# Performance work log

Hardware: AMD Instinct MI355X
Metric: run time of the kernel (lower is better)

Reference implementation:

```python
import jax, jax.numpy as jnp
import numpy as np

B, S, H, E, K, D = 1, 4096, 1024, 8, 2, 2048

def setup_inputs() -> dict:
    key = jax.random.key(0)
    k1, k2, k3, k4, k5 = jax.random.split(key, 5)
    x = jax.random.normal(k1, (B, S, H), dtype=jnp.float32)
    attention_mask = jnp.ones((B, S), dtype=jnp.int32)
    expert_weights = jax.random.uniform(k2, (B, S, K), dtype=jnp.float32)
    # distinct top-K expert indices per token (torch code requires at most one match per token)
    r = jax.random.uniform(k3, (B, S, E))
    chosen_expert_indices = jnp.argsort(r, axis=-1)[..., :K].astype(jnp.int64)
    down_proj = jax.random.normal(k4, (E, H, D), dtype=jnp.float32)
    up_proj = jax.random.normal(k5, (E, D, H), dtype=jnp.float32)
    return {"x": x, "attention_mask": attention_mask, "expert_weights": expert_weights,
            "chosen_expert_indices": chosen_expert_indices, "down_proj": down_proj, "up_proj": up_proj}

def reference(x, attention_mask, expert_weights, chosen_expert_indices, down_proj, up_proj):
    b, s, h = x.shape
    e = down_proj.shape[0]
    xt = x.reshape(-1, h)                                   # [N,H]
    n = xt.shape[0]
    mask = attention_mask.reshape(n, 1).astype(x.dtype)     # [N,1]
    idx = chosen_expert_indices.reshape(n, -1)              # [N,K]
    w = expert_weights.reshape(n, -1)                       # [N,K]
    onehot = jax.nn.one_hot(idx, e, dtype=x.dtype)          # [N,K,E]
    # per-token routing weight for each expert (0 if not chosen), masked
    we = jnp.einsum('nk,nke->ne', w, onehot) * mask         # [N,E]
    hid = jax.nn.relu(jnp.einsum('nh,ehd->end', xt, down_proj))  # [E,N,D]
    y = jnp.einsum('end,edh->enh', hid, up_proj)            # [E,N,H]
    mlp = jnp.einsum('ne,enh->nh', we, y)                   # [N,H]
    out = xt + mlp                                          # residual (B==1 as in source)
    return out.reshape(b, s, h)
```

## Files before the change

kernel.cpp:

```cpp
#include <hip/hip_runtime.h>
#include <stdint.h>

#define NTOK 4096
#define HDIM 1024
#define DDIM 2048
#define NEXP 8
#define NASS 8192

typedef __attribute__((ext_vector_type(8))) short bf16x8;
typedef __attribute__((ext_vector_type(4))) float f32x4;

typedef __attribute__((address_space(1))) const unsigned int gu32;
typedef __attribute__((address_space(3))) unsigned int lu32;

#define BARRIER() asm volatile("s_barrier" ::: "memory")
#define WAIT_VM0() asm volatile("s_waitcnt vmcnt(0)" ::: "memory")
#define WAIT_LGKM0() do { asm volatile("s_waitcnt lgkmcnt(0)" ::: "memory"); \
                          __builtin_amdgcn_sched_barrier(0); } while (0)

__device__ __forceinline__ void async16(void* lds, const void* g) {
  __builtin_amdgcn_global_load_lds((gu32*)(uintptr_t)g, (lu32*)(uintptr_t)lds, 16, 0, 0);
}

__device__ __forceinline__ unsigned short f2bf(float f) {
  unsigned int u = __float_as_uint(f);
  return (unsigned short)((u + 0x7fffu + ((u >> 16) & 1u)) >> 16);
}
__device__ __forceinline__ float bf2f(unsigned short u) {
  return __uint_as_float(((unsigned int)u) << 16);
}
__device__ __forceinline__ unsigned int pack2(float lo, float hi) {
  return (unsigned int)f2bf(lo) | ((unsigned int)f2bf(hi) << 16);
}

__device__ __forceinline__ void transpose128(const float* __restrict__ in,
                                             unsigned short* __restrict__ out,
                                             int R, int C, int e, int bk, int bn,
                                             float* tile, int tid) {
  const size_t mbase = (size_t)e * R * C;
#pragma unroll
  for (int it = 0; it < 16; ++it) {
    int row = it * 8 + (tid >> 5);
    int c4 = (tid & 31) * 4;
    float4 v = *reinterpret_cast<const float4*>(
        in + mbase + (size_t)(bk * 128 + row) * C + bn * 128 + c4);
    tile[row * 129 + c4 + 0] = v.x; tile[row * 129 + c4 + 1] = v.y;
    tile[row * 129 + c4 + 2] = v.z; tile[row * 129 + c4 + 3] = v.w;
  }
  __syncthreads();
#pragma unroll
  for (int it = 0; it < 8; ++it) {
    int n = it * 16 + (tid >> 4);
    int k8 = (tid & 15) * 8;
    uint4 o;
    o.x = pack2(tile[(k8 + 0) * 129 + n], tile[(k8 + 1) * 129 + n]);
    o.y = pack2(tile[(k8 + 2) * 129 + n], tile[(k8 + 3) * 129 + n]);
    o.z = pack2(tile[(k8 + 4) * 129 + n], tile[(k8 + 5) * 129 + n]);
    o.w = pack2(tile[(k8 + 6) * 129 + n], tile[(k8 + 7) * 129 + n]);
    *reinterpret_cast<uint4*>(out + mbase + (size_t)(bn * 128 + n) * R + bk * 128 + k8) = o;
  }
}

__global__ __launch_bounds__(256) void k_prep(
    const float* __restrict__ x, unsigned short* __restrict__ x16,
    const float* __restrict__ dn, unsigned short* __restrict__ dnT,
    const float* __restrict__ up, unsigned short* __restrict__ upT) {
  __shared__ float tile[128 * 129];
  const int b = blockIdx.x;
  const int tid = threadIdx.x;
  if (b < 1024) {
    int e = b >> 7, t = b & 127;
    transpose128(dn, dnT, HDIM, DDIM, e, t & 7, t >> 3, tile, tid);
  } else if (b < 2048) {
    int idx = b - 1024;
    int e = idx >> 7, t = idx & 127;
    transpose128(up, upT, DDIM, HDIM, e, t & 15, t >> 4, tile, tid);
  } else {
    int i = (b - 2048) * 2048 + tid * 8;
    float4 v0 = *reinterpret_cast<const float4*>(x + i);
    float4 v1 = *reinterpret_cast<const float4*>(x + i + 4);
    uint4 o;
    o.x = pack2(v0.x, v0.y); o.y = pack2(v0.z, v0.w);
    o.z = pack2(v1.x, v1.y); o.w = pack2(v1.z, v1.w);
    *reinterpret_cast<uint4*>(x16 + i) = o;
  }
}

__global__ __launch_bounds__(1024) void k_route(
    const int* __restrict__ idx, const float* __restrict__ ew,
    const int* __restrict__ amask,
    int* __restrict__ counts_g, int* __restrict__ offs_g,
    int* __restrict__ toks, float* __restrict__ wl, int* __restrict__ slotmap) {
  __shared__ int cnt[NEXP], cur[NEXP], flag;
  const int t = threadIdx.x;
  if (t < NEXP) cnt[t] = 0;
  if (t == 0) flag = 0;
  __syncthreads();
  int lf = 0;
#pragma unroll
  for (int j = 0; j < 4; ++j) {
    int i = t + j * 1024;
    if (idx[2 * i + 1] != 0) lf = 1;
  }
  if (lf) atomicOr(&flag, 1);
  __syncthreads();
  const int is32 = flag;
  int e[8];
#pragma unroll
  for (int j = 0; j < 8; ++j) {
    int i = t + j * 1024;
    int ei = is32 ? idx[i] : idx[2 * i];
    e[j] = ei;
    atomicAdd(&cnt[ei], 1);
  }
  __syncthreads();
  if (t == 0) {
    int off = 0;
    for (int k = 0; k < NEXP; ++k) {
      cur[k] = off; offs_g[k] = off; counts_g[k] = cnt[k]; off += cnt[k];
    }
  }
  __syncthreads();
#pragma unroll
  for (int j = 0; j < 8; ++j) {
    int i = t + j * 1024;
    int n = i >> 1;
    int slot = atomicAdd(&cur[e[j]], 1);
    toks[slot] = n;
    wl[slot] = ew[i] * (amask[n] ? 1.0f : 0.0f);
    slotmap[i] = slot;
  }
}

__global__ __launch_bounds__(256, 4) void k_gemm_down(
    const unsigned short* __restrict__ x16, const unsigned short* __restrict__ bT,
    const int* __restrict__ counts, const int* __restrict__ offs,
    const int* __restrict__ toks, unsigned short* __restrict__ hid) {
  const int e = blockIdx.x;
  const int cnt = counts[e];
  const int q = blockIdx.y;
  const int mt = q >> 4;
  const int nt = q & 15;
  if (mt * 128 >= cnt) return;
  const int base = offs[e];
  __shared__ alignas(16) char lds[65536];
  const int tid = threadIdx.x;
  const int lane = tid & 63;
  const int wr = ((tid >> 7) & 1) * 64;
  const int wc = ((tid >> 6) & 1) * 64;

  const char* gA[4]; const char* gB[4]; int sOff[4];
  {
    const int swcol = ((tid & 7) << 4) ^ (((tid >> 3) & 7) << 4);
#pragma unroll
    for (int s = 0; s < 4; ++s) {
      int row = s * 32 + (tid >> 3);
      int sl = mt * 128 + row; if (sl >= cnt) sl = cnt - 1;
      gA[s] = (const char*)(x16 + (size_t)toks[base + sl] * HDIM) + swcol;
      gB[s] = (const char*)(bT + (size_t)e * DDIM * HDIM + (size_t)(nt * 128 + row) * HDIM) + swcol;
      sOff[s] = s * 4096 + tid * 16;
    }
  }
  const int swz = (lane & 7) << 4;
  const int lo = (lane >> 4) << 4;
  int rowA[4], rowB[4];
#pragma unroll
  for (int m = 0; m < 4; ++m) rowA[m] = (wr + m * 16 + (lane & 15)) * 128;
#pragma unroll
  for (int n = 0; n < 4; ++n) rowB[n] = (wc + n * 16 + (lane & 15)) * 128;

#pragma unroll
  for (int s = 0; s < 4; ++s) {
    async16(lds + sOff[s], gA[s]);
    async16(lds + 32768 + sOff[s], gB[s]);
  }

  f32x4 acc[4][4] = {};
  for (int j = 0; j < 16; ++j) {
    WAIT_VM0();
    BARRIER();
    char* curA = lds + ((j & 1) << 14);
    char* curB = lds + 32768 + ((j & 1) << 14);
    if (j < 15) {
      const int ko = (j + 1) << 7;
      char* nA = lds + ((~j & 1) << 14);
      char* nB = lds + 32768 + ((~j & 1) << 14);
#pragma unroll
      for (int s = 0; s < 4; ++s) {
        async16(nA + sOff[s], gA[s] + ko);
        async16(nB + sOff[s], gB[s] + ko);
      }
    }
#pragma unroll
    for (int ks = 0; ks < 2; ++ks) {
      const int cx = ((ks << 6) | lo) ^ swz;
      bf16x8 fa[4], fb[4];
#pragma unroll
      for (int n = 0; n < 4; ++n) fb[n] = *reinterpret_cast<const bf16x8*>(curB + rowB[n] + cx);
#pragma unroll
      for (int m = 0; m < 4; ++m) fa[m] = *reinterpret_cast<const bf16x8*>(curA + rowA[m] + cx);
      WAIT_LGKM0();
      __builtin_amdgcn_s_setprio(1);
#pragma unroll
      for (int m = 0; m < 4; ++m)
#pragma unroll
        for (int n = 0; n < 4; ++n)
          acc[m][n] = __builtin_amdgcn_mfma_f32_16x16x32_bf16(fa[m], fb[n], acc[m][n], 0, 0, 0);
      __builtin_amdgcn_s_setprio(0);
    }
  }

#pragma unroll
  for (int m = 0; m < 4; ++m) {
    int r0 = mt * 128 + wr + m * 16 + ((lane >> 4) * 4);
#pragma unroll
    for (int jj = 0; jj < 4; ++jj) {
      int r = r0 + jj;
      if (r < cnt) {
        unsigned short* dst = hid + (size_t)(base + r) * DDIM + nt * 128 + wc + (lane & 15);
#pragma unroll
        for (int n = 0; n < 4; ++n) {
          float v = acc[m][n][jj];
          dst[n * 16] = f2bf(v > 0.f ? v : 0.f);
        }
      }
    }
  }
}

__global__ __launch_bounds__(256, 4) void k_gemm_up(
    const unsigned short* __restrict__ hid, const unsigned short* __restrict__ bT,
    const int* __restrict__ counts, const int* __restrict__ offs,
    unsigned short* __restrict__ yw) {
  const int e = blockIdx.x;
  const int cnt = counts[e];
  const int q = blockIdx.y;
  const int mt = q >> 3;
  const int nt = q & 7;
  if (mt * 128 >= cnt) return;
  const int base = offs[e];
  __shared__ alignas(16) char lds[65536];
  const int tid = threadIdx.x;
  const int lane = tid & 63;
  const int wr = ((tid >> 7) & 1) * 64;
  const int wc = ((tid >> 6) & 1) * 64;

  const char* gA[4]; const char* gB[4]; int sOff[4];
  {
    const int swcol = ((tid & 7) << 4) ^ (((tid >> 3) & 7) << 4);
#pragma unroll
    for (int s = 0; s < 4; ++s) {
      int row = s * 32 + (tid >> 3);
      int sl = mt * 128 + row; if (sl >= cnt) sl = cnt - 1;
      gA[s] = (const char*)(hid + (size_t)(base + sl) * DDIM) + swcol;
      gB[s] = (const char*)(bT + (size_t)e * HDIM * DDIM + (size_t)(nt * 128 + row) * DDIM) + swcol;
      sOff[s] = s * 4096 + tid * 16;
    }
  }
  const int swz = (lane & 7) << 4;
  const int lo = (lane >> 4) << 4;
  int rowA[4], rowB[4];
#pragma unroll
  for (int m = 0; m < 4; ++m) rowA[m] = (wr + m * 16 + (lane & 15)) * 128;
#pragma unroll
  for (int n = 0; n < 4; ++n) rowB[n] = (wc + n * 16 + (lane & 15)) * 128;

#pragma unroll
  for (int s = 0; s < 4; ++s) {
    async16(lds + sOff[s], gA[s]);
    async16(lds + 32768 + sOff[s], gB[s]);
  }

  f32x4 acc[4][4] = {};
  for (int j = 0; j < 32; ++j) {
    WAIT_VM0();
    BARRIER();
    char* curA = lds + ((j & 1) << 14);
    char* curB = lds + 32768 + ((j & 1) << 14);
    if (j < 31) {
      const int ko = (j + 1) << 7;
      char* nA = lds + ((~j & 1) << 14);
      char* nB = lds + 32768 + ((~j & 1) << 14);
#pragma unroll
      for (int s = 0; s < 4; ++s) {
        async16(nA + sOff[s], gA[s] + ko);
        async16(nB + sOff[s], gB[s] + ko);
      }
    }
#pragma unroll
    for (int ks = 0; ks < 2; ++ks) {
      const int cx = ((ks << 6) | lo) ^ swz;
      bf16x8 fa[4], fb[4];
#pragma unroll
      for (int n = 0; n < 4; ++n) fb[n] = *reinterpret_cast<const bf16x8*>(curB + rowB[n] + cx);
#pragma unroll
      for (int m = 0; m < 4; ++m) fa[m] = *reinterpret_cast<const bf16x8*>(curA + rowA[m] + cx);
      WAIT_LGKM0();
      __builtin_amdgcn_s_setprio(1);
#pragma unroll
      for (int m = 0; m < 4; ++m)
#pragma unroll
        for (int n = 0; n < 4; ++n)
          acc[m][n] = __builtin_amdgcn_mfma_f32_16x16x32_bf16(fa[m], fb[n], acc[m][n], 0, 0, 0);
      __builtin_amdgcn_s_setprio(0);
    }
  }

#pragma unroll
  for (int m = 0; m < 4; ++m) {
    int r0 = mt * 128 + wr + m * 16 + ((lane >> 4) * 4);
#pragma unroll
    for (int jj = 0; jj < 4; ++jj) {
      int r = r0 + jj;
      if (r < cnt) {
        unsigned short* dst = yw + (size_t)(base + r) * HDIM + nt * 128 + wc + (lane & 15);
#pragma unroll
        for (int n = 0; n < 4; ++n) dst[n * 16] = f2bf(acc[m][n][jj]);
      }
    }
  }
}

__global__ __launch_bounds__(256) void k_combine(
    const float* __restrict__ x, const unsigned short* __restrict__ yw,
    const int* __restrict__ slotmap, const float* __restrict__ wl,
    float* __restrict__ out) {
  const int n = blockIdx.x;
  const int t = threadIdx.x;
  const int s0 = slotmap[2 * n], s1 = slotmap[2 * n + 1];
  const float w0 = wl[s0], w1 = wl[s1];
  float4 xv = reinterpret_cast<const float4*>(x + (size_t)n * HDIM)[t];
  ushort4 a0 = reinterpret_cast<const ushort4*>(yw + (size_t)s0 * HDIM)[t];
  ushort4 b0 = reinterpret_cast<const ushort4*>(yw + (size_t)s1 * HDIM)[t];
  float4 r;
  r.x = xv.x + w0 * bf2f(a0.x) + w1 * bf2f(b0.x);
  r.y = xv.y + w0 * bf2f(a0.y) + w1 * bf2f(b0.y);
  r.z = xv.z + w0 * bf2f(a0.z) + w1 * bf2f(b0.z);
  r.w = xv.w + w0 * bf2f(a0.w) + w1 * bf2f(b0.w);
  reinterpret_cast<float4*>(out + (size_t)n * HDIM)[t] = r;
}

extern "C" void kernel_launch(void* const* d_in, const int* in_sizes, int n_in,
                              void* d_out, int out_size, void* d_ws, size_t ws_size,
                              hipStream_t stream) {
  const float* x    = (const float*)d_in[0];
  const int* amask  = (const int*)d_in[1];
  const float* ew   = (const float*)d_in[2];
  const int* cidx   = (const int*)d_in[3];
  const float* dn   = (const float*)d_in[4];
  const float* up   = (const float*)d_in[5];
  float* out        = (float*)d_out;
  char* ws          = (char*)d_ws;

  const size_t X16_OFF = 0;
  const size_t DNT_OFF = X16_OFF + (size_t)NTOK * HDIM * 2;
  const size_t UPT_OFF = DNT_OFF + (size_t)NEXP * HDIM * DDIM * 2;
  const size_t HID_OFF = UPT_OFF + (size_t)NEXP * HDIM * DDIM * 2;
  const size_t MET_OFF = HID_OFF + (size_t)NASS * DDIM * 2;

  unsigned short* x16 = (unsigned short*)(ws + X16_OFF);
  unsigned short* dnT = (unsigned short*)(ws + DNT_OFF);
  unsigned short* upT = (unsigned short*)(ws + UPT_OFF);
  unsigned short* hid = (unsigned short*)(ws + HID_OFF);
  unsigned short* yw  = (unsigned short*)(ws + DNT_OFF);
  int* counts  = (int*)(ws + MET_OFF);
  int* offs    = counts + 8;
  int* toks    = counts + 32;
  float* wl    = (float*)(toks + NASS);
  int* slotmap = (int*)(wl + NASS);

  k_prep<<<1024 + 1024 + 2048, 256, 0, stream>>>(x, x16, dn, dnT, up, upT);
  k_route<<<1, 1024, 0, stream>>>(cidx, ew, amask, counts, offs, toks, wl, slotmap);
  k_gemm_down<<<dim3(8, 1024), 256, 0, stream>>>(x16, dnT, counts, offs, toks, hid);
  k_gemm_up<<<dim3(8, 512), 256, 0, stream>>>(hid, upT, counts, offs, yw);
  k_combine<<<NTOK, 256, 0, stream>>>(x, yw, slotmap, wl, out);
}
```

Measured before the change: 147.2 us.

## Fuse fp32 weight transpose and bf16 conversion into the expert GEMM B-tile loads

Removes the separate prep pass that transposed and converted both expert weight tensors to bf16. Each GEMM block now reads fp32 weights straight from global memory into registers, converts them to bf16 and writes them transposed into swizzled LDS, prefetching two K-tiles ahead. This saves a full pass over the weights and the matching workspace traffic. In exchange, fp32 weights are re-read by every M-tile block (twice the bytes of bf16), the strided per-column loads are less efficient than the old async LDS copies, and occupancy drops from 4 to 2 blocks per CU because of the extra registers.

```diff
diff --git a/kernel.cpp b/kernel.cpp
--- a/kernel.cpp
+++ b/kernel.cpp
@@ -33,57 +33,15 @@
   return (unsigned int)f2bf(lo) | ((unsigned int)f2bf(hi) << 16);
 }
 
-__device__ __forceinline__ void transpose128(const float* __restrict__ in,
-                                             unsigned short* __restrict__ out,
-                                             int R, int C, int e, int bk, int bn,
-                                             float* tile, int tid) {
-  const size_t mbase = (size_t)e * R * C;
-#pragma unroll
-  for (int it = 0; it < 16; ++it) {
-    int row = it * 8 + (tid >> 5);
-    int c4 = (tid & 31) * 4;
-    float4 v = *reinterpret_cast<const float4*>(
-        in + mbase + (size_t)(bk * 128 + row) * C + bn * 128 + c4);
-    tile[row * 129 + c4 + 0] = v.x; tile[row * 129 + c4 + 1] = v.y;
-    tile[row * 129 + c4 + 2] = v.z; tile[row * 129 + c4 + 3] = v.w;
-  }
-  __syncthreads();
-#pragma unroll
-  for (int it = 0; it < 8; ++it) {
-    int n = it * 16 + (tid >> 4);
-    int k8 = (tid & 15) * 8;
-    uint4 o;
-    o.x = pack2(tile[(k8 + 0) * 129 + n], tile[(k8 + 1) * 129 + n]);
-    o.y = pack2(tile[(k8 + 2) * 129 + n], tile[(k8 + 3) * 129 + n]);
-    o.z = pack2(tile[(k8 + 4) * 129 + n], tile[(k8 + 5) * 129 + n]);
-    o.w = pack2(tile[(k8 + 6) * 129 + n], tile[(k8 + 7) * 129 + n]);
-    *reinterpret_cast<uint4*>(out + mbase + (size_t)(bn * 128 + n) * R + bk * 128 + k8) = o;
-  }
-}
-
-__global__ __launch_bounds__(256) void k_prep(
-    const float* __restrict__ x, unsigned short* __restrict__ x16,
-    const float* __restrict__ dn, unsigned short* __restrict__ dnT,
-    const float* __restrict__ up, unsigned short* __restrict__ upT) {
-  __shared__ float tile[128 * 129];
-  const int b = blockIdx.x;
-  const int tid = threadIdx.x;
-  if (b < 1024) {
-    int e = b >> 7, t = b & 127;
-    transpose128(dn, dnT, HDIM, DDIM, e, t & 7, t >> 3, tile, tid);
-  } else if (b < 2048) {
-    int idx = b - 1024;
-    int e = idx >> 7, t = idx & 127;
-    transpose128(up, upT, DDIM, HDIM, e, t & 15, t >> 4, tile, tid);
-  } else {
-    int i = (b - 2048) * 2048 + tid * 8;
-    float4 v0 = *reinterpret_cast<const float4*>(x + i);
-    float4 v1 = *reinterpret_cast<const float4*>(x + i + 4);
-    uint4 o;
-    o.x = pack2(v0.x, v0.y); o.y = pack2(v0.z, v0.w);
-    o.z = pack2(v1.x, v1.y); o.w = pack2(v1.z, v1.w);
-    *reinterpret_cast<uint4*>(x16 + i) = o;
-  }
+__global__ __launch_bounds__(256) void k_cvt_x(const float* __restrict__ x,
+                                               unsigned short* __restrict__ x16) {
+  int i = blockIdx.x * 2048 + threadIdx.x * 8;
+  float4 v0 = *reinterpret_cast<const float4*>(x + i);
+  float4 v1 = *reinterpret_cast<const float4*>(x + i + 4);
+  uint4 o;
+  o.x = pack2(v0.x, v0.y); o.y = pack2(v0.z, v0.w);
+  o.z = pack2(v1.x, v1.y); o.w = pack2(v1.z, v1.w);
+  *reinterpret_cast<uint4*>(x16 + i) = o;
 }
 
 __global__ __launch_bounds__(1024) void k_route(
@@ -132,8 +90,8 @@
   }
 }
 
-__global__ __launch_bounds__(256, 4) void k_gemm_down(
-    const unsigned short* __restrict__ x16, const unsigned short* __restrict__ bT,
+__global__ __launch_bounds__(256, 2) void k_gemm_down(
+    const unsigned short* __restrict__ x16, const float* __restrict__ dn,
     const int* __restrict__ counts, const int* __restrict__ offs,
     const int* __restrict__ toks, unsigned short* __restrict__ hid) {
   const int e = blockIdx.x;
@@ -149,7 +107,7 @@
   const int wr = ((tid >> 7) & 1) * 64;
   const int wc = ((tid >> 6) & 1) * 64;
 
-  const char* gA[4]; const char* gB[4]; int sOff[4];
+  const char* gA[4]; int sOff[4];
   {
     const int swcol = ((tid & 7) << 4) ^ (((tid >> 3) & 7) << 4);
 #pragma unroll
@@ -157,10 +115,17 @@
       int row = s * 32 + (tid >> 3);
       int sl = mt * 128 + row; if (sl >= cnt) sl = cnt - 1;
       gA[s] = (const char*)(x16 + (size_t)toks[base + sl] * HDIM) + swcol;
-      gB[s] = (const char*)(bT + (size_t)e * DDIM * HDIM + (size_t)(nt * 128 + row) * HDIM) + swcol;
       sOff[s] = s * 4096 + tid * 16;
     }
   }
+  const int nloc = tid & 127;
+  const int kc0 = __builtin_amdgcn_readfirstlane((tid >> 7) << 3);
+  const float* bw = dn + (size_t)e * HDIM * DDIM + nt * 128 + nloc;
+  int bOff[4];
+#pragma unroll
+  for (int c = 0; c < 4; ++c)
+    bOff[c] = nloc * 128 + (((kc0 + c * 16) * 2) ^ ((nloc & 7) << 4));
+
   const int swz = (lane & 7) << 4;
   const int lo = (lane >> 4) << 4;
   int rowA[4], rowB[4];
@@ -169,11 +134,25 @@
 #pragma unroll
   for (int n = 0; n < 4; ++n) rowB[n] = (wc + n * 16 + (lane & 15)) * 128;
 
-#pragma unroll
-  for (int s = 0; s < 4; ++s) {
-    async16(lds + sOff[s], gA[s]);
-    async16(lds + 32768 + sOff[s], gB[s]);
-  }
+  float bv[4][8];
+#define LOADB_DN(jt) do { \
+  _Pragma("unroll") for (int c = 0; c < 4; ++c) \
+    _Pragma("unroll") for (int jj = 0; jj < 8; ++jj) \
+      bv[c][jj] = bw[(size_t)((jt) * 64 + kc0 + c * 16 + jj) * DDIM]; } while (0)
+#define STOREB(dst) do { \
+  _Pragma("unroll") for (int c = 0; c < 4; ++c) { \
+    uint4 o; \
+    o.x = pack2(bv[c][0], bv[c][1]); o.y = pack2(bv[c][2], bv[c][3]); \
+    o.z = pack2(bv[c][4], bv[c][5]); o.w = pack2(bv[c][6], bv[c][7]); \
+    *reinterpret_cast<uint4*>((dst) + bOff[c]) = o; } } while (0)
+
+  LOADB_DN(0);
+  WAIT_VM0();
+  STOREB(lds + 32768);
+#pragma unroll
+  for (int s = 0; s < 4; ++s) async16(lds + sOff[s], gA[s]);
+  LOADB_DN(1);
+  asm volatile("s_waitcnt lgkmcnt(0)" ::: "memory");
 
   f32x4 acc[4][4] = {};
   for (int j = 0; j < 16; ++j) {
@@ -182,15 +161,13 @@
     char* curA = lds + ((j & 1) << 14);
     char* curB = lds + 32768 + ((j & 1) << 14);
     if (j < 15) {
-      const int ko = (j + 1) << 7;
       char* nA = lds + ((~j & 1) << 14);
       char* nB = lds + 32768 + ((~j & 1) << 14);
-#pragma unroll
-      for (int s = 0; s < 4; ++s) {
-        async16(nA + sOff[s], gA[s] + ko);
-        async16(nB + sOff[s], gB[s] + ko);
-      }
-    }
+      STOREB(nB);
+#pragma unroll
+      for (int s = 0; s < 4; ++s) async16(nA + sOff[s], gA[s] + (j + 1) * 128);
+    }
+    if (j < 14) LOADB_DN(j + 2);
 #pragma unroll
     for (int ks = 0; ks < 2; ++ks) {
       const int cx = ((ks << 6) | lo) ^ swz;
@@ -226,10 +203,12 @@
       }
     }
   }
-}
-
-__global__ __launch_bounds__(256, 4) void k_gemm_up(
-    const unsigned short* __restrict__ hid, const unsigned short* __restrict__ bT,
+#undef LOADB_DN
+#undef STOREB
+}
+
+__global__ __launch_bounds__(256, 2) void k_gemm_up(
+    const unsigned short* __restrict__ hid, const float* __restrict__ up,
     const int* __restrict__ counts, const int* __restrict__ offs,
     unsigned short* __restrict__ yw) {
   const int e = blockIdx.x;
@@ -245,7 +224,7 @@
   const int wr = ((tid >> 7) & 1) * 64;
   const int wc = ((tid >> 6) & 1) * 64;
 
-  const char* gA[4]; const char* gB[4]; int sOff[4];
+  const char* gA[4]; int sOff[4];
   {
     const int swcol = ((tid & 7) << 4) ^ (((tid >> 3) & 7) << 4);
 #pragma unroll
@@ -253,10 +232,17 @@
       int row = s * 32 + (tid >> 3);
       int sl = mt * 128 + row; if (sl >= cnt) sl = cnt - 1;
       gA[s] = (const char*)(hid + (size_t)(base + sl) * DDIM) + swcol;
-      gB[s] = (const char*)(bT + (size_t)e * HDIM * DDIM + (size_t)(nt * 128 + row) * DDIM) + swcol;
       sOff[s] = s * 4096 + tid * 16;
     }
   }
+  const int nloc = tid & 127;
+  const int kc0 = __builtin_amdgcn_readfirstlane((tid >> 7) << 3);
+  const float* bw = up + (size_t)e * DDIM * HDIM + nt * 128 + nloc;
+  int bOff[4];
+#pragma unroll
+  for (int c = 0; c < 4; ++c)
+    bOff[c] = nloc * 128 + (((kc0 + c * 16) * 2) ^ ((nloc & 7) << 4));
+
   const int swz = (lane & 7) << 4;
   const int lo = (lane >> 4) << 4;
   int rowA[4], rowB[4];
@@ -265,11 +251,25 @@
 #pragma unroll
   for (int n = 0; n < 4; ++n) rowB[n] = (wc + n * 16 + (lane & 15)) * 128;
 
-#pragma unroll
-  for (int s = 0; s < 4; ++s) {
-    async16(lds + sOff[s], gA[s]);
-    async16(lds + 32768 + sOff[s], gB[s]);
-  }
+  float bv[4][8];
+#define LOADB_UP(jt) do { \
+  _Pragma("unroll") for (int c = 0; c < 4; ++c) \
+    _Pragma("unroll") for (int jj = 0; jj < 8; ++jj) \
+      bv[c][jj] = bw[(size_t)((jt) * 64 + kc0 + c * 16 + jj) * HDIM]; } while (0)
+#define STOREB(dst) do { \
+  _Pragma("unroll") for (int c = 0; c < 4; ++c) { \
+    uint4 o; \
+    o.x = pack2(bv[c][0], bv[c][1]); o.y = pack2(bv[c][2], bv[c][3]); \
+    o.z = pack2(bv[c][4], bv[c][5]); o.w = pack2(bv[c][6], bv[c][7]); \
+    *reinterpret_cast<uint4*>((dst) + bOff[c]) = o; } } while (0)
+
+  LOADB_UP(0);
+  WAIT_VM0();
+  STOREB(lds + 32768);
+#pragma unroll
+  for (int s = 0; s < 4; ++s) async16(lds + sOff[s], gA[s]);
+  LOADB_UP(1);
+  asm volatile("s_waitcnt lgkmcnt(0)" ::: "memory");
 
   f32x4 acc[4][4] = {};
   for (int j = 0; j < 32; ++j) {
@@ -278,15 +278,13 @@
     char* curA = lds + ((j & 1) << 14);
     char* curB = lds + 32768 + ((j & 1) << 14);
     if (j < 31) {
-      const int ko = (j + 1) << 7;
       char* nA = lds + ((~j & 1) << 14);
       char* nB = lds + 32768 + ((~j & 1) << 14);
-#pragma unroll
-      for (int s = 0; s < 4; ++s) {
-        async16(nA + sOff[s], gA[s] + ko);
-        async16(nB + sOff[s], gB[s] + ko);
-      }
-    }
+      STOREB(nB);
+#pragma unroll
+      for (int s = 0; s < 4; ++s) async16(nA + sOff[s], gA[s] + (j + 1) * 128);
+    }
+    if (j < 30) LOADB_UP(j + 2);
 #pragma unroll
     for (int ks = 0; ks < 2; ++ks) {
       const int cx = ((ks << 6) | lo) ^ swz;
@@ -319,6 +317,8 @@
       }
     }
   }
+#undef LOADB_UP
+#undef STOREB
 }
 
 __global__ __launch_bounds__(256) void k_combine(
@@ -353,25 +353,22 @@
   char* ws          = (char*)d_ws;
 
   const size_t X16_OFF = 0;
-  const size_t DNT_OFF = X16_OFF + (size_t)NTOK * HDIM * 2;
-  const size_t UPT_OFF = DNT_OFF + (size_t)NEXP * HDIM * DDIM * 2;
-  const size_t HID_OFF = UPT_OFF + (size_t)NEXP * HDIM * DDIM * 2;
-  const size_t MET_OFF = HID_OFF + (size_t)NASS * DDIM * 2;
+  const size_t HID_OFF = X16_OFF + (size_t)NTOK * HDIM * 2;
+  const size_t YW_OFF  = HID_OFF + (size_t)NASS * DDIM * 2;
+  const size_t MET_OFF = YW_OFF  + (size_t)NASS * HDIM * 2;
 
   unsigned short* x16 = (unsigned short*)(ws + X16_OFF);
-  unsigned short* dnT = (unsigned short*)(ws + DNT_OFF);
-  unsigned short* upT = (unsigned short*)(ws + UPT_OFF);
   unsigned short* hid = (unsigned short*)(ws + HID_OFF);
-  unsigned short* yw  = (unsigned short*)(ws + DNT_OFF);
+  unsigned short* yw  = (unsigned short*)(ws + YW_OFF);
   int* counts  = (int*)(ws + MET_OFF);
   int* offs    = counts + 8;
   int* toks    = counts + 32;
   float* wl    = (float*)(toks + NASS);
   int* slotmap = (int*)(wl + NASS);
 
-  k_prep<<<1024 + 1024 + 2048, 256, 0, stream>>>(x, x16, dn, dnT, up, upT);
+  k_cvt_x<<<NTOK * HDIM / 2048, 256, 0, stream>>>(x, x16);
   k_route<<<1, 1024, 0, stream>>>(cidx, ew, amask, counts, offs, toks, wl, slotmap);
-  k_gemm_down<<<dim3(8, 1024), 256, 0, stream>>>(x16, dnT, counts, offs, toks, hid);
-  k_gemm_up<<<dim3(8, 512), 256, 0, stream>>>(hid, upT, counts, offs, yw);
+  k_gemm_down<<<dim3(8, 1024), 256, 0, stream>>>(x16, dn, counts, offs, toks, hid);
+  k_gemm_up<<<dim3(8, 512), 256, 0, stream>>>(hid, up, counts, offs, yw);
   k_combine<<<NTOK, 256, 0, stream>>>(x, yw, slotmap, wl, out);
 }
```

New measurement: 177.7 us. 1.21x slower.

## Fold routing into prep kernel and fix transpose write coalescing

Applied to the files above, without the earlier changes.

Removes the separate single-block routing kernel and runs routing as one extra block of the prep kernel, which drops a launch and lets routing overlap with the weight transposes. The transpose output loop also swaps its thread mapping so that consecutive threads vary n instead of k8. That changes both the LDS read pattern and the global store pattern. Routing now runs on 256 threads instead of 1024, with 32 entries per thread, so that single block does more serial work and holds more registers.

```diff
diff --git a/kernel.cpp b/kernel.cpp
--- a/kernel.cpp
+++ b/kernel.cpp
@@ -48,10 +48,10 @@
     tile[row * 129 + c4 + 2] = v.z; tile[row * 129 + c4 + 3] = v.w;
   }
   __syncthreads();
+  const int k8 = (tid >> 4) * 8;
 #pragma unroll
   for (int it = 0; it < 8; ++it) {
-    int n = it * 16 + (tid >> 4);
-    int k8 = (tid & 15) * 8;
+    int n = it * 16 + (tid & 15);
     uint4 o;
     o.x = pack2(tile[(k8 + 0) * 129 + n], tile[(k8 + 1) * 129 + n]);
     o.y = pack2(tile[(k8 + 2) * 129 + n], tile[(k8 + 3) * 129 + n]);
@@ -64,7 +64,11 @@
 __global__ __launch_bounds__(256) void k_prep(
     const float* __restrict__ x, unsigned short* __restrict__ x16,
     const float* __restrict__ dn, unsigned short* __restrict__ dnT,
-    const float* __restrict__ up, unsigned short* __restrict__ upT) {
+    const float* __restrict__ up, unsigned short* __restrict__ upT,
+    const int* __restrict__ idx, const float* __restrict__ ew,
+    const int* __restrict__ amask,
+    int* __restrict__ counts_g, int* __restrict__ offs_g,
+    int* __restrict__ toks, float* __restrict__ wl, int* __restrict__ slotmap) {
   __shared__ float tile[128 * 129];
   const int b = blockIdx.x;
   const int tid = threadIdx.x;
@@ -72,10 +76,10 @@
     int e = b >> 7, t = b & 127;
     transpose128(dn, dnT, HDIM, DDIM, e, t & 7, t >> 3, tile, tid);
   } else if (b < 2048) {
-    int idx = b - 1024;
-    int e = idx >> 7, t = idx & 127;
+    int i2 = b - 1024;
+    int e = i2 >> 7, t = i2 & 127;
     transpose128(up, upT, DDIM, HDIM, e, t & 15, t >> 4, tile, tid);
-  } else {
+  } else if (b < 4096) {
     int i = (b - 2048) * 2048 + tid * 8;
     float4 v0 = *reinterpret_cast<const float4*>(x + i);
     float4 v1 = *reinterpret_cast<const float4*>(x + i + 4);
@@ -83,52 +87,45 @@
     o.x = pack2(v0.x, v0.y); o.y = pack2(v0.z, v0.w);
     o.z = pack2(v1.x, v1.y); o.w = pack2(v1.z, v1.w);
     *reinterpret_cast<uint4*>(x16 + i) = o;
-  }
-}
-
-__global__ __launch_bounds__(1024) void k_route(
-    const int* __restrict__ idx, const float* __restrict__ ew,
-    const int* __restrict__ amask,
-    int* __restrict__ counts_g, int* __restrict__ offs_g,
-    int* __restrict__ toks, float* __restrict__ wl, int* __restrict__ slotmap) {
-  __shared__ int cnt[NEXP], cur[NEXP], flag;
-  const int t = threadIdx.x;
-  if (t < NEXP) cnt[t] = 0;
-  if (t == 0) flag = 0;
-  __syncthreads();
-  int lf = 0;
-#pragma unroll
-  for (int j = 0; j < 4; ++j) {
-    int i = t + j * 1024;
-    if (idx[2 * i + 1] != 0) lf = 1;
-  }
-  if (lf) atomicOr(&flag, 1);
-  __syncthreads();
-  const int is32 = flag;
-  int e[8];
-#pragma unroll
-  for (int j = 0; j < 8; ++j) {
-    int i = t + j * 1024;
-    int ei = is32 ? idx[i] : idx[2 * i];
-    e[j] = ei;
-    atomicAdd(&cnt[ei], 1);
-  }
-  __syncthreads();
-  if (t == 0) {
-    int off = 0;
-    for (int k = 0; k < NEXP; ++k) {
-      cur[k] = off; offs_g[k] = off; counts_g[k] = cnt[k]; off += cnt[k];
-    }
-  }
-  __syncthreads();
-#pragma unroll
-  for (int j = 0; j < 8; ++j) {
-    int i = t + j * 1024;
-    int n = i >> 1;
-    int slot = atomicAdd(&cur[e[j]], 1);
-    toks[slot] = n;
-    wl[slot] = ew[i] * (amask[n] ? 1.0f : 0.0f);
-    slotmap[i] = slot;
+  } else {
+    int* ishm = (int*)tile;
+    if (tid < NEXP) ishm[tid] = 0;
+    if (tid == 8) ishm[16] = 0;
+    __syncthreads();
+    int lf = 0;
+#pragma unroll
+    for (int j = 0; j < 16; ++j) {
+      int i = tid + j * 256;
+      if (idx[2 * i + 1] != 0) lf = 1;
+    }
+    if (lf) atomicOr(&ishm[16], 1);
+    __syncthreads();
+    const int is32 = ishm[16];
+    int e[32];
+#pragma unroll
+    for (int j = 0; j < 32; ++j) {
+      int i = tid + j * 256;
+      int ei = is32 ? idx[i] : idx[2 * i];
+      e[j] = ei;
+      atomicAdd(&ishm[ei], 1);
+    }
+    __syncthreads();
+    if (tid == 0) {
+      int off = 0;
+      for (int k = 0; k < NEXP; ++k) {
+        ishm[8 + k] = off; offs_g[k] = off; counts_g[k] = ishm[k]; off += ishm[k];
+      }
+    }
+    __syncthreads();
+#pragma unroll
+    for (int j = 0; j < 32; ++j) {
+      int i = tid + j * 256;
+      int n = i >> 1;
+      int slot = atomicAdd(&ishm[8 + e[j]], 1);
+      toks[slot] = n;
+      wl[slot] = ew[i] * (amask[n] ? 1.0f : 0.0f);
+      slotmap[i] = slot;
+    }
   }
 }
 
@@ -369,8 +366,8 @@
   float* wl    = (float*)(toks + NASS);
   int* slotmap = (int*)(wl + NASS);
 
-  k_prep<<<1024 + 1024 + 2048, 256, 0, stream>>>(x, x16, dn, dnT, up, upT);
-  k_route<<<1, 1024, 0, stream>>>(cidx, ew, amask, counts, offs, toks, wl, slotmap);
+  k_prep<<<4097, 256, 0, stream>>>(x, x16, dn, dnT, up, upT,
+                                   cidx, ew, amask, counts, offs, toks, wl, slotmap);
   k_gemm_down<<<dim3(8, 1024), 256, 0, stream>>>(x16, dnT, counts, offs, toks, hid);
   k_gemm_up<<<dim3(8, 512), 256, 0, stream>>>(hid, upT, counts, offs, yw);
   k_combine<<<NTOK, 256, 0, stream>>>(x, yw, slotmap, wl, out);
```

Measured after the change: 152.8 us. 1.04x slower.
